# Kernel tuning notes

Measured on AMD Instinct MI355X. Metric: run time of the kernel, lower is better.

## Reference

```python
import jax, jax.numpy as jnp
import numpy as np

N_NODES = 100000
N_EDGES = 3200000
D_FEAT = 32


def setup_inputs() -> dict:
    key = jax.random.key(0)
    k1, k2, k3 = jax.random.split(key, 3)
    inp = jax.random.normal(k1, (N_NODES, D_FEAT), dtype=jnp.float32)
    eidx = jax.random.randint(k2, (2, N_EDGES), 0, N_NODES, dtype=jnp.int64)
    enorm = jax.random.uniform(k3, (N_EDGES,), dtype=jnp.float32)
    esgn = jnp.ones((N_EDGES,), dtype=jnp.float32)
    return {"input": inp, "eidx": eidx, "enorm": enorm, "esgn": esgn}


def reference(input, eidx, enorm, esgn):
    # Gather source node features, scale by sign * norm, scatter-add to targets.
    sidx, tidx = eidx[0], eidx[1]
    message = input[sidx] * (esgn * enorm)[:, None]  # [n_edges, d]
    res = jax.ops.segment_sum(message, tidx, num_segments=input.shape[0])
    return res.astype(input.dtype)
```

## Files before the change

kernel.cpp:

```cpp
#include <hip/hip_runtime.h>


#define G    256
#define KMAX 1024
#define SPAN_SHIFT 7
#define SPAN 128
#define CAP  6144
#define NB   256

__global__ __launch_bounds__(1024) void hist_kernel(
    const int* __restrict__ tidx, int* __restrict__ cnt,
    int n_edges, int epb, int vec)
{
    __shared__ int lh[KMAX];
    int g = blockIdx.x, t = threadIdx.x;
    lh[t] = 0;
    __syncthreads();
    int beg = g * epb;
    int lim = beg + epb; if (lim > n_edges) lim = n_edges;
    if (vec) {
        int nq = (lim > beg) ? ((lim - beg) >> 2) : 0;
        for (int q = t; q < nq; q += 1024) {
            int4 tn = *(const int4*)(tidx + beg + q * 4);
            atomicAdd(&lh[tn.x >> SPAN_SHIFT], 1);
            atomicAdd(&lh[tn.y >> SPAN_SHIFT], 1);
            atomicAdd(&lh[tn.z >> SPAN_SHIFT], 1);
            atomicAdd(&lh[tn.w >> SPAN_SHIFT], 1);
        }
        for (int e = beg + (nq << 2) + t; e < lim; e += 1024)
            atomicAdd(&lh[tidx[e] >> SPAN_SHIFT], 1);
    } else {
        for (int e = beg + t; e < lim; e += 1024)
            atomicAdd(&lh[tidx[e] >> SPAN_SHIFT], 1);
    }
    __syncthreads();
    cnt[g * KMAX + t] = lh[t];
}

__global__ __launch_bounds__(G) void scan1_kernel(
    const int* __restrict__ cnt, int* __restrict__ pref, int* __restrict__ tot)
{
    __shared__ int part[G];
    int b = blockIdx.x, t = threadIdx.x;
    int c = cnt[t * KMAX + b];
    part[t] = c;
    __syncthreads();
    for (int off = 1; off < G; off <<= 1) {
        int v = (t >= off) ? part[t - off] : 0;
        __syncthreads();
        part[t] += v;
        __syncthreads();
    }
    pref[t * KMAX + b] = part[t] - c;
    if (t == G - 1) tot[b] = part[t];
}

__global__ __launch_bounds__(1024) void scatter_kernel(
    const int* __restrict__ sidx, const int* __restrict__ tidx,
    const float* __restrict__ enorm, const float* __restrict__ esgn,
    const int* __restrict__ tot, const int* __restrict__ pref,
    int2* __restrict__ recs, int n_edges, int epb, int vec)
{
    __shared__ int gbase[KMAX];
    __shared__ int lh[KMAX];
    __shared__ int part[KMAX];
    int g = blockIdx.x, t = threadIdx.x;

    int c = tot[t];
    part[t] = c;
    __syncthreads();
    for (int off = 1; off < KMAX; off <<= 1) {
        int v = (t >= off) ? part[t - off] : 0;
        __syncthreads();
        part[t] += v;
        __syncthreads();
    }
    gbase[t] = (part[t] - c) + pref[g * KMAX + t];
    lh[t] = 0;
    __syncthreads();

    int beg = g * epb;
    int lim = beg + epb; if (lim > n_edges) lim = n_edges;

    #define SCAT_EDGE(tn_, sn_, w_) {                                        \
        int b_ = (tn_) >> SPAN_SHIFT;                                        \
        int rank_ = atomicAdd(&lh[b_], 1);                                   \
        unsigned rec_ = ((unsigned)(sn_) << SPAN_SHIFT) |                    \
                        (unsigned)((tn_) & (SPAN - 1));                      \
        recs[gbase[b_] + rank_] = make_int2((int)rec_, __float_as_int(w_)); }

    if (vec) {
        int nq = (lim > beg) ? ((lim - beg) >> 2) : 0;
        for (int q = t; q < nq; q += 1024) {
            int e = beg + q * 4;
            int4   tn = *(const int4*)(tidx + e);
            int4   sn = *(const int4*)(sidx + e);
            float4 nw = *(const float4*)(enorm + e);
            float4 sw = *(const float4*)(esgn + e);
            SCAT_EDGE(tn.x, sn.x, nw.x * sw.x);
            SCAT_EDGE(tn.y, sn.y, nw.y * sw.y);
            SCAT_EDGE(tn.z, sn.z, nw.z * sw.z);
            SCAT_EDGE(tn.w, sn.w, nw.w * sw.w);
        }
        for (int e = beg + (nq << 2) + t; e < lim; e += 1024) {
            int tn = tidx[e]; int sn = sidx[e];
            float w = enorm[e] * esgn[e];
            SCAT_EDGE(tn, sn, w);
        }
    } else {
        for (int e = beg + t; e < lim; e += 1024) {
            int tn = tidx[e]; int sn = sidx[e];
            float w = enorm[e] * esgn[e];
            SCAT_EDGE(tn, sn, w);
        }
    }
    #undef SCAT_EDGE
}

__global__ __launch_bounds__(1024) void bucket_accum(
    const float* __restrict__ input, const int2* __restrict__ recs,
    const int* __restrict__ tot, float* __restrict__ out, int n_nodes)
{
    __shared__ int2 srec[CAP];
    __shared__ int part[KMAX];
    __shared__ int lcnt[SPAN];
    __shared__ int lbeg[SPAN];
    __shared__ int lcur[SPAN];
    __shared__ int sb[2];
    int b = blockIdx.x;
    int t = threadIdx.x;

    int c = tot[t];
    part[t] = c;
    __syncthreads();
    for (int off = 1; off < KMAX; off <<= 1) {
        int v = (t >= off) ? part[t - off] : 0;
        __syncthreads();
        part[t] += v;
        __syncthreads();
    }
    if (t == b) { sb[0] = part[t] - c; sb[1] = part[t]; }
    __syncthreads();
    int bstart = sb[0], bend = sb[1];
    int base_node = b << SPAN_SHIFT;

    if (bend - bstart <= CAP) {
        if (t < SPAN) lcnt[t] = 0;
        __syncthreads();
        for (int i = bstart + t; i < bend; i += 1024)
            atomicAdd(&lcnt[recs[i].x & (SPAN - 1)], 1);
        __syncthreads();
        int cc = (t < SPAN) ? lcnt[t] : 0;
        if (t < SPAN) lbeg[t] = cc;
        __syncthreads();
        for (int off = 1; off < SPAN; off <<= 1) {
            int v = (t < SPAN && t >= off) ? lbeg[t - off] : 0;
            __syncthreads();
            if (t < SPAN) lbeg[t] += v;
            __syncthreads();
        }
        if (t < SPAN) {
            int excl = lbeg[t] - cc;
            lbeg[t] = excl;
            lcur[t] = excl;
        }
        __syncthreads();
        for (int i = bstart + t; i < bend; i += 1024) {
            int2 r = recs[i];
            int pos = atomicAdd(&lcur[r.x & (SPAN - 1)], 1);
            srec[pos] = r;
        }
        __syncthreads();
        int node = t >> 3;
        int lane = t & 7;
        int beg = lbeg[node];
        int end = beg + lcnt[node];
        float4 acc = make_float4(0.f, 0.f, 0.f, 0.f);
        int i = beg;
        for (; i + 3 < end; i += 4) {
            int2 q0 = srec[i];
            int2 q1 = srec[i + 1];
            int2 q2 = srec[i + 2];
            int2 q3 = srec[i + 3];
            float4 v0 = ((const float4*)(input + (size_t)(((unsigned)q0.x) >> SPAN_SHIFT) * 32))[lane];
            float4 v1 = ((const float4*)(input + (size_t)(((unsigned)q1.x) >> SPAN_SHIFT) * 32))[lane];
            float4 v2 = ((const float4*)(input + (size_t)(((unsigned)q2.x) >> SPAN_SHIFT) * 32))[lane];
            float4 v3 = ((const float4*)(input + (size_t)(((unsigned)q3.x) >> SPAN_SHIFT) * 32))[lane];
            float w0 = __int_as_float(q0.y);
            float w1 = __int_as_float(q1.y);
            float w2 = __int_as_float(q2.y);
            float w3 = __int_as_float(q3.y);
            acc.x = fmaf(w0, v0.x, acc.x);
            acc.y = fmaf(w0, v0.y, acc.y);
            acc.z = fmaf(w0, v0.z, acc.z);
            acc.w = fmaf(w0, v0.w, acc.w);
            acc.x = fmaf(w1, v1.x, acc.x);
            acc.y = fmaf(w1, v1.y, acc.y);
            acc.z = fmaf(w1, v1.z, acc.z);
            acc.w = fmaf(w1, v1.w, acc.w);
            acc.x = fmaf(w2, v2.x, acc.x);
            acc.y = fmaf(w2, v2.y, acc.y);
            acc.z = fmaf(w2, v2.z, acc.z);
            acc.w = fmaf(w2, v2.w, acc.w);
            acc.x = fmaf(w3, v3.x, acc.x);
            acc.y = fmaf(w3, v3.y, acc.y);
            acc.z = fmaf(w3, v3.z, acc.z);
            acc.w = fmaf(w3, v3.w, acc.w);
        }
        for (; i < end; ++i) {
            int2 q = srec[i];
            float w = __int_as_float(q.y);
            float4 v = ((const float4*)(input + (size_t)(((unsigned)q.x) >> SPAN_SHIFT) * 32))[lane];
            acc.x = fmaf(w, v.x, acc.x);
            acc.y = fmaf(w, v.y, acc.y);
            acc.z = fmaf(w, v.z, acc.z);
            acc.w = fmaf(w, v.w, acc.w);
        }
        int gnode = base_node + node;
        if (gnode < n_nodes)
            ((float4*)(out + (size_t)gnode * 32))[lane] = acc;
    } else {
        for (int i = t; i < SPAN * 32; i += 1024) {
            int gn = base_node + (i >> 5);
            if (gn < n_nodes) out[(size_t)gn * 32 + (i & 31)] = 0.f;
        }
        __syncthreads();
        for (int i = bstart + t; i < bend; i += 1024) {
            int2 r = recs[i];
            float w = __int_as_float(r.y);
            int s = (int)(((unsigned)r.x) >> SPAN_SHIFT);
            int gn = base_node + (r.x & (SPAN - 1));
            if (gn < n_nodes)
                for (int j = 0; j < 32; ++j)
                    atomicAdd(&out[(size_t)gn * 32 + j], w * input[(size_t)s * 32 + j]);
        }
    }
}

__global__ __launch_bounds__(NB) void graphconv_scatter(
    const float* __restrict__ input, const int* __restrict__ sidx,
    const int* __restrict__ tidx, const float* __restrict__ enorm,
    const float* __restrict__ esgn, float* __restrict__ out, int n_edges)
{
    int t = blockIdx.x * NB + threadIdx.x;
    int e = t >> 3;
    int sub = t & 7;
    if (e >= n_edges) return;
    int s = sidx[e];
    int d = tidx[e];
    float w = enorm[e] * esgn[e];
    const float4* src = (const float4*)(input + (size_t)s * 32);
    float4 v = src[sub];
    float* op = out + (size_t)d * 32 + sub * 4;
    atomicAdd(op + 0, v.x * w);
    atomicAdd(op + 1, v.y * w);
    atomicAdd(op + 2, v.z * w);
    atomicAdd(op + 3, v.w * w);
}

extern "C" void kernel_launch(void* const* d_in, const int* in_sizes, int n_in,
                              void* d_out, int out_size, void* d_ws, size_t ws_size,
                              hipStream_t stream) {
    const float* input = (const float*)d_in[0];
    const int*   eidx  = (const int*)d_in[1];
    const float* enorm = (const float*)d_in[2];
    const float* esgn  = (const float*)d_in[3];
    float*       out   = (float*)d_out;

    int n_edges = in_sizes[1] / 2;
    int n_nodes = in_sizes[0] / 32;
    const int* sidx = eidx;
    const int* tidx = eidx + n_edges;

    int K = (n_nodes + SPAN - 1) >> SPAN_SHIFT;

    size_t need = (size_t)n_edges * 8 +
                  ((size_t)2 * G * KMAX + KMAX) * 4;

    if (ws_size >= need && K <= KMAX) {
        int2* recs  = (int2*)d_ws;
        int*  cnt   = (int*)(recs + n_edges);
        int*  pref  = cnt + (size_t)G * KMAX;
        int*  tot   = pref + (size_t)G * KMAX;

        int epb = ((n_edges + G - 1) / G + 3) & ~3;
        int vec = ((n_edges & 3) == 0 &&
                   (((uintptr_t)tidx | (uintptr_t)sidx |
                     (uintptr_t)enorm | (uintptr_t)esgn) & 15) == 0) ? 1 : 0;

        hist_kernel   <<<G,    1024, 0, stream>>>(tidx, cnt, n_edges, epb, vec);
        scan1_kernel  <<<KMAX, G,    0, stream>>>(cnt, pref, tot);
        scatter_kernel<<<G,    1024, 0, stream>>>(sidx, tidx, enorm, esgn,
                                                  tot, pref, recs,
                                                  n_edges, epb, vec);
        bucket_accum  <<<K,    1024, 0, stream>>>(input, recs, tot,
                                                  out, n_nodes);
    } else {
        hipMemsetAsync(d_out, 0, (size_t)out_size * sizeof(float), stream);
        size_t threads_total = (size_t)n_edges * 8;
        int grid = (int)((threads_total + NB - 1) / NB);
        graphconv_scatter<<<grid, NB, 0, stream>>>(input, sidx, tidx, enorm, esgn,
                                                   out, n_edges);
    }
}
```

Before: 198.2 us.

## Fold per-block prefix scan into scatter kernel and unroll gather loop by eight

Drops the separate scan1 kernel launch. Each scatter block now computes its own exclusive prefix over the 256 histogram rows with a serial loop, reading the count matrix directly, and block 0 writes the bucket totals. This removes one launch and the pref buffer, but every block now redundantly reads the whole count matrix (256 KB per block). The accumulate kernel's gather loop also gains an 8-way unrolled path so more independent float4 loads are in flight.

```diff
diff --git a/kernel.cpp b/kernel.cpp
--- a/kernel.cpp
+++ b/kernel.cpp
@@ -37,28 +37,10 @@
     cnt[g * KMAX + t] = lh[t];
 }
 
-__global__ __launch_bounds__(G) void scan1_kernel(
-    const int* __restrict__ cnt, int* __restrict__ pref, int* __restrict__ tot)
-{
-    __shared__ int part[G];
-    int b = blockIdx.x, t = threadIdx.x;
-    int c = cnt[t * KMAX + b];
-    part[t] = c;
-    __syncthreads();
-    for (int off = 1; off < G; off <<= 1) {
-        int v = (t >= off) ? part[t - off] : 0;
-        __syncthreads();
-        part[t] += v;
-        __syncthreads();
-    }
-    pref[t * KMAX + b] = part[t] - c;
-    if (t == G - 1) tot[b] = part[t];
-}
-
 __global__ __launch_bounds__(1024) void scatter_kernel(
     const int* __restrict__ sidx, const int* __restrict__ tidx,
     const float* __restrict__ enorm, const float* __restrict__ esgn,
-    const int* __restrict__ tot, const int* __restrict__ pref,
+    const int* __restrict__ cnt, int* __restrict__ tot,
     int2* __restrict__ recs, int n_edges, int epb, int vec)
 {
     __shared__ int gbase[KMAX];
@@ -66,8 +48,13 @@
     __shared__ int part[KMAX];
     int g = blockIdx.x, t = threadIdx.x;
 
-    int c = tot[t];
-    part[t] = c;
+    int run = 0, my = 0;
+    for (int gp = 0; gp < G; ++gp) {
+        if (gp == g) my = run;
+        run += cnt[gp * KMAX + t];
+    }
+    if (g == 0) tot[t] = run;
+    part[t] = run;
     __syncthreads();
     for (int off = 1; off < KMAX; off <<= 1) {
         int v = (t >= off) ? part[t - off] : 0;
@@ -75,7 +62,7 @@
         part[t] += v;
         __syncthreads();
     }
-    gbase[t] = (part[t] - c) + pref[g * KMAX + t];
+    gbase[t] = (part[t] - run) + my;
     lh[t] = 0;
     __syncthreads();
 
@@ -177,45 +164,41 @@
         int end = beg + lcnt[node];
         float4 acc = make_float4(0.f, 0.f, 0.f, 0.f);
         int i = beg;
+
+        #define GAT1(qq)                                                     \
+            float4 v##qq = ((const float4*)(input +                          \
+                (size_t)(((unsigned)q##qq.x) >> SPAN_SHIFT) * 32))[lane];    \
+            float w##qq = __int_as_float(q##qq.y);
+        #define FMA1(qq)                                                     \
+            acc.x = fmaf(w##qq, v##qq.x, acc.x);                             \
+            acc.y = fmaf(w##qq, v##qq.y, acc.y);                             \
+            acc.z = fmaf(w##qq, v##qq.z, acc.z);                             \
+            acc.w = fmaf(w##qq, v##qq.w, acc.w);
+
+        for (; i + 7 < end; i += 8) {
+            int2 q0 = srec[i];     int2 q1 = srec[i + 1];
+            int2 q2 = srec[i + 2]; int2 q3 = srec[i + 3];
+            int2 q4 = srec[i + 4]; int2 q5 = srec[i + 5];
+            int2 q6 = srec[i + 6]; int2 q7 = srec[i + 7];
+            GAT1(0) GAT1(1) GAT1(2) GAT1(3)
+            GAT1(4) GAT1(5) GAT1(6) GAT1(7)
+            FMA1(0) FMA1(1) FMA1(2) FMA1(3)
+            FMA1(4) FMA1(5) FMA1(6) FMA1(7)
+        }
         for (; i + 3 < end; i += 4) {
+            int2 q0 = srec[i];     int2 q1 = srec[i + 1];
+            int2 q2 = srec[i + 2]; int2 q3 = srec[i + 3];
+            GAT1(0) GAT1(1) GAT1(2) GAT1(3)
+            FMA1(0) FMA1(1) FMA1(2) FMA1(3)
+        }
+        for (; i < end; ++i) {
             int2 q0 = srec[i];
-            int2 q1 = srec[i + 1];
-            int2 q2 = srec[i + 2];
-            int2 q3 = srec[i + 3];
-            float4 v0 = ((const float4*)(input + (size_t)(((unsigned)q0.x) >> SPAN_SHIFT) * 32))[lane];
-            float4 v1 = ((const float4*)(input + (size_t)(((unsigned)q1.x) >> SPAN_SHIFT) * 32))[lane];
-            float4 v2 = ((const float4*)(input + (size_t)(((unsigned)q2.x) >> SPAN_SHIFT) * 32))[lane];
-            float4 v3 = ((const float4*)(input + (size_t)(((unsigned)q3.x) >> SPAN_SHIFT) * 32))[lane];
-            float w0 = __int_as_float(q0.y);
-            float w1 = __int_as_float(q1.y);
-            float w2 = __int_as_float(q2.y);
-            float w3 = __int_as_float(q3.y);
-            acc.x = fmaf(w0, v0.x, acc.x);
-            acc.y = fmaf(w0, v0.y, acc.y);
-            acc.z = fmaf(w0, v0.z, acc.z);
-            acc.w = fmaf(w0, v0.w, acc.w);
-            acc.x = fmaf(w1, v1.x, acc.x);
-            acc.y = fmaf(w1, v1.y, acc.y);
-            acc.z = fmaf(w1, v1.z, acc.z);
-            acc.w = fmaf(w1, v1.w, acc.w);
-            acc.x = fmaf(w2, v2.x, acc.x);
-            acc.y = fmaf(w2, v2.y, acc.y);
-            acc.z = fmaf(w2, v2.z, acc.z);
-            acc.w = fmaf(w2, v2.w, acc.w);
-            acc.x = fmaf(w3, v3.x, acc.x);
-            acc.y = fmaf(w3, v3.y, acc.y);
-            acc.z = fmaf(w3, v3.z, acc.z);
-            acc.w = fmaf(w3, v3.w, acc.w);
-        }
-        for (; i < end; ++i) {
-            int2 q = srec[i];
-            float w = __int_as_float(q.y);
-            float4 v = ((const float4*)(input + (size_t)(((unsigned)q.x) >> SPAN_SHIFT) * 32))[lane];
-            acc.x = fmaf(w, v.x, acc.x);
-            acc.y = fmaf(w, v.y, acc.y);
-            acc.z = fmaf(w, v.z, acc.z);
-            acc.w = fmaf(w, v.w, acc.w);
-        }
+            GAT1(0)
+            FMA1(0)
+        }
+        #undef GAT1
+        #undef FMA1
+
         int gnode = base_node + node;
         if (gnode < n_nodes)
             ((float4*)(out + (size_t)gnode * 32))[lane] = acc;
@@ -275,13 +258,12 @@
     int K = (n_nodes + SPAN - 1) >> SPAN_SHIFT;
 
     size_t need = (size_t)n_edges * 8 +
-                  ((size_t)2 * G * KMAX + KMAX) * 4;
+                  ((size_t)G * KMAX + KMAX) * 4;
 
     if (ws_size >= need && K <= KMAX) {
         int2* recs  = (int2*)d_ws;
         int*  cnt   = (int*)(recs + n_edges);
-        int*  pref  = cnt + (size_t)G * KMAX;
-        int*  tot   = pref + (size_t)G * KMAX;
+        int*  tot   = cnt + (size_t)G * KMAX;
 
         int epb = ((n_edges + G - 1) / G + 3) & ~3;
         int vec = ((n_edges & 3) == 0 &&
@@ -289,9 +271,8 @@
                      (uintptr_t)enorm | (uintptr_t)esgn) & 15) == 0) ? 1 : 0;
 
         hist_kernel   <<<G,    1024, 0, stream>>>(tidx, cnt, n_edges, epb, vec);
-        scan1_kernel  <<<KMAX, G,    0, stream>>>(cnt, pref, tot);
         scatter_kernel<<<G,    1024, 0, stream>>>(sidx, tidx, enorm, esgn,
-                                                  tot, pref, recs,
+                                                  cnt, tot, recs,
                                                   n_edges, epb, vec);
         bucket_accum  <<<K,    1024, 0, stream>>>(input, recs, tot,
                                                   out, n_nodes);
```

After: 208.7 us. 1.05x slower.
